# Kernel tuning notes

Measured on AMD Instinct MI355X. Metric: run time of the kernel, lower is better.

Reference implementation:

```python
import jax, jax.numpy as jnp
import numpy as np

B, S, D, H = 4, 2048, 1024, 16
HD = D // H  # 64
EPS = 1e-6


def _layernorm(x, scale, bias):
    mu = jnp.mean(x, axis=-1, keepdims=True)
    var = jnp.mean(jnp.square(x - mu), axis=-1, keepdims=True)
    return (x - mu) * jax.lax.rsqrt(var + EPS) * scale + bias


def setup_inputs() -> dict:
    key = jax.random.key(0)
    ks = jax.random.split(key, 10)
    s = 0.02
    return {
        "x": jax.random.normal(ks[0], (B, S, D), jnp.float32),
        "attention_mask": jnp.ones((B, 1, S, S), jnp.bool_),
        "eval": 1,
        "Wq": jax.random.normal(ks[1], (D, D), jnp.float32) * s,
        "bq": jnp.zeros((D,), jnp.float32),
        "Wk": jax.random.normal(ks[2], (D, D), jnp.float32) * s,
        "bk": jnp.zeros((D,), jnp.float32),
        "Wv": jax.random.normal(ks[3], (D, D), jnp.float32) * s,
        "bv": jnp.zeros((D,), jnp.float32),
        "Wo": jax.random.normal(ks[4], (D, D), jnp.float32) * s,
        "bo": jnp.zeros((D,), jnp.float32),
        "W1": jax.random.normal(ks[5], (D, D), jnp.float32) * s,
        "b1": jnp.zeros((D,), jnp.float32),
        "W2": jax.random.normal(ks[6], (D, D), jnp.float32) * s,
        "b2": jnp.zeros((D,), jnp.float32),
        "ln1_scale": jnp.ones((D,), jnp.float32),
        "ln1_bias": jnp.zeros((D,), jnp.float32),
        "ln2_scale": jnp.ones((D,), jnp.float32),
        "ln2_bias": jnp.zeros((D,), jnp.float32),
    }


def reference(x, attention_mask, eval, Wq, bq, Wk, bk, Wv, bv, Wo, bo,
              W1, b1, W2, b2, ln1_scale, ln1_bias, ln2_scale, ln2_bias):
    # --- MultiHeadAttention ---
    q = (x @ Wq + bq).reshape(B, S, H, HD)
    k = (x @ Wk + bk).reshape(B, S, H, HD)
    v = (x @ Wv + bv).reshape(B, S, H, HD)
    scores = jnp.einsum('bqhd,bkhd->bhqk', q, k) / jnp.sqrt(jnp.float32(HD))
    scores = jnp.where(attention_mask, scores, -jnp.inf)
    attn = jax.nn.softmax(scores, axis=-1)
    vals = jnp.einsum('bhqk,bkhd->bqhd', attn, v).reshape(B, S, D)
    attn_out = vals @ Wo + bo
    # --- residual + LN ---
    h = _layernorm(x + attn_out, ln1_scale, ln1_bias)
    # --- FeedForward (dropout deterministic -> identity) ---
    ff = jnp.maximum(h @ W1 + b1, 0.0) @ W2 + b2
    return _layernorm(h + ff, ln2_scale, ln2_bias)
```

## Files before the change

### kernel.cpp

```cpp
#include <hip/hip_runtime.h>

typedef __bf16 bf16;
typedef __bf16 bf16x8 __attribute__((ext_vector_type(8)));
typedef __bf16 bf16x4 __attribute__((ext_vector_type(4)));
typedef float f32x4 __attribute__((ext_vector_type(4)));
typedef float f32x16 __attribute__((ext_vector_type(16)));
typedef unsigned int uint;

#define BB 4
#define SS 2048
#define DD 1024
#define HH 16
#define HD 64
#define GM 8192
#define GN 1024
#define GK 1024
#define KVB 64
#define NT (SS / KVB)

__device__ __forceinline__ f32x4 mfma16(bf16x8 a, bf16x8 b, f32x4 c) {
    return __builtin_amdgcn_mfma_f32_16x16x32_bf16(a, b, c, 0, 0, 0);
}
__device__ __forceinline__ f32x16 mfma32(bf16x8 a, bf16x8 b, f32x16 c) {
    return __builtin_amdgcn_mfma_f32_32x32x16_bf16(a, b, c, 0, 0, 0);
}
__device__ __forceinline__ uint pack2(float x, float y) {
    union { bf16 b[2]; uint u; } uu;
    uu.b[0] = (bf16)x; uu.b[1] = (bf16)y;
    return uu.u;
}

__global__ __launch_bounds__(256) void cvt_kernel(const float* __restrict__ in, bf16* __restrict__ out, int n4) {
    int i = blockIdx.x * 256 + threadIdx.x;
    if (i < n4) {
        float4 v = *(const float4*)(in + (size_t)i * 4);
        bf16x4 o = {(bf16)v.x, (bf16)v.y, (bf16)v.z, (bf16)v.w};
        *(bf16x4*)(out + (size_t)i * 4) = o;
    }
}

__global__ __launch_bounds__(256) void wtrans_kernel(const float* __restrict__ W, bf16* __restrict__ Wt) {
    __shared__ float tile[64][65];
    const int t = threadIdx.x;
    const int k0 = blockIdx.x * 64, n0 = blockIdx.y * 64;
#pragma unroll
    for (int i = 0; i < 16; ++i) {
        int idx = i * 256 + t;
        int r = idx >> 6, c = idx & 63;
        tile[r][c] = W[(size_t)(k0 + r) * DD + n0 + c];
    }
    __syncthreads();
#pragma unroll
    for (int i = 0; i < 16; ++i) {
        int idx = i * 256 + t;
        int r = idx >> 6, c = idx & 63;
        Wt[(size_t)(n0 + r) * DD + k0 + c] = (bf16)tile[c][r];
    }
}

__global__ __launch_bounds__(256) void vtrans_kernel(const bf16* __restrict__ V, bf16* __restrict__ Vt) {
    __shared__ bf16 tile[64][72];
    const int t = threadIdx.x;
    const int bh = blockIdx.y;
    const int b = bh >> 4, h = bh & 15;
    const int s0 = blockIdx.x * 64;
#pragma unroll
    for (int i = 0; i < 16; ++i) {
        int idx = i * 256 + t;
        int r = idx >> 6, c = idx & 63;
        tile[r][c] = V[(size_t)(b * SS + s0 + r) * DD + h * HD + c];
    }
    __syncthreads();
#pragma unroll
    for (int i = 0; i < 16; ++i) {
        int idx = i * 256 + t;
        int r = idx >> 6, c = idx & 63;
        Vt[((size_t)bh * HD + r) * SS + s0 + c] = tile[c][r];
    }
}

template<bool OUTBF, bool RELU>
__global__ __launch_bounds__(256) void gemm_bt(const bf16* __restrict__ A, const bf16* __restrict__ Bt,
                                               const float* __restrict__ bias, void* __restrict__ C) {
    const int m0 = blockIdx.x * 128;
    const int n0 = blockIdx.y * 128;
    const int t = threadIdx.x;
    const int l = t & 63, wid = t >> 6;
    const int l16 = l & 15, g = l >> 4;
    const int wr = wid >> 1, wc = wid & 1;

    __shared__ int4 As4[512];
    __shared__ int4 Bs4[512];
    const char* Asc = (const char*)As4;
    const char* Bsc = (const char*)Bs4;

    const bf16* pa = A + (size_t)(m0 + (t >> 2)) * GK + (t & 3) * 8;
    const bf16* pb = Bt + (size_t)(n0 + (t >> 2)) * GK + (t & 3) * 8;
    int4 ra0 = *(const int4*)pa;
    int4 ra1 = *(const int4*)(pa + 64 * GK);
    int4 rb0 = *(const int4*)pb;
    int4 rb1 = *(const int4*)(pb + 64 * GK);

    f32x4 z = {0.f, 0.f, 0.f, 0.f};
    f32x4 acc[4][4];
#pragma unroll
    for (int mi = 0; mi < 4; ++mi)
#pragma unroll
        for (int ni = 0; ni < 4; ++ni) acc[mi][ni] = z;

    for (int kt = 0; kt < GK / 32; ++kt) {
        __syncthreads();
        As4[t] = ra0; As4[t + 256] = ra1;
        Bs4[t] = rb0; Bs4[t + 256] = rb1;
        __syncthreads();
        if (kt < GK / 32 - 1) {
            int off = (kt + 1) * 32;
            ra0 = *(const int4*)(pa + off);
            ra1 = *(const int4*)(pa + 64 * GK + off);
            rb0 = *(const int4*)(pb + off);
            rb1 = *(const int4*)(pb + 64 * GK + off);
        }
        bf16x8 af[4], bfr[4];
#pragma unroll
        for (int mi = 0; mi < 4; ++mi)
            af[mi] = *(const bf16x8*)(Asc + ((wr * 64 + mi * 16 + l16) * 32 + g * 8) * 2);
#pragma unroll
        for (int ni = 0; ni < 4; ++ni)
            bfr[ni] = *(const bf16x8*)(Bsc + ((wc * 64 + ni * 16 + l16) * 32 + g * 8) * 2);
#pragma unroll
        for (int mi = 0; mi < 4; ++mi)
#pragma unroll
            for (int ni = 0; ni < 4; ++ni)
                acc[mi][ni] = mfma16(af[mi], bfr[ni], acc[mi][ni]);
    }
#pragma unroll
    for (int ni = 0; ni < 4; ++ni) {
        const int col = n0 + wc * 64 + ni * 16 + l16;
        const float bv = bias[col];
#pragma unroll
        for (int mi = 0; mi < 4; ++mi) {
            const int row0 = m0 + wr * 64 + mi * 16 + g * 4;
#pragma unroll
            for (int j = 0; j < 4; ++j) {
                float v = acc[mi][ni][j] + bv;
                if (RELU) v = fmaxf(v, 0.f);
                if (OUTBF) ((bf16*)C)[(size_t)(row0 + j) * GN + col] = (bf16)v;
                else       ((float*)C)[(size_t)(row0 + j) * GN + col] = v;
            }
        }
    }
}

#define PFRAG(P, OFF, DST) { \
    uint a0 = pack2(P[OFF + 0], P[OFF + 1]); \
    uint a1 = pack2(P[OFF + 2], P[OFF + 3]); \
    uint a2 = pack2(P[OFF + 4], P[OFF + 5]); \
    uint a3 = pack2(P[OFF + 6], P[OFF + 7]); \
    uint s0 = (uint)__shfl_xor((int)a0, 32); \
    uint s1 = (uint)__shfl_xor((int)a1, 32); \
    uint s2 = (uint)__shfl_xor((int)a2, 32); \
    uint s3 = (uint)__shfl_xor((int)a3, 32); \
    union { uint u[4]; bf16x8 v; } uu; \
    uu.u[0] = lh ? s2 : a0; \
    uu.u[1] = lh ? s3 : a1; \
    uu.u[2] = lh ? a2 : s0; \
    uu.u[3] = lh ? a3 : s1; \
    DST = uu.v; }

__global__ __launch_bounds__(512) void attn_kernel(const bf16* __restrict__ Q, const bf16* __restrict__ K,
                                                   const bf16* __restrict__ Vt, bf16* __restrict__ vals) {
    const int wg = blockIdx.x;
    const int bh = wg >> 3;
    const int b = bh >> 4, h = bh & 15;
    const int q0 = (wg & 7) << 8;
    const int t = threadIdx.x;
    const int w = t >> 6, l = t & 63;
    const int l31 = l & 31, lh = l >> 5;
    const int qrow = q0 + w * 32 + l31;

    __shared__ int4 lds4[2048];
    char* lds = (char*)lds4;

    const float QS = 0.125f * 1.44269504f;
    const bf16* qp = Q + ((size_t)(b * SS + qrow)) * DD + h * HD + lh * 8;
    bf16x8 qf[4];
#pragma unroll
    for (int dc = 0; dc < 4; ++dc) {
        bf16x8 v = *(const bf16x8*)(qp + dc * 16);
#pragma unroll
        for (int j = 0; j < 8; ++j) v[j] = (bf16)((float)v[j] * QS);
        qf[dc] = v;
    }

    const int srow = t >> 3, schunk = t & 7;
    const bf16* kgp = K + ((size_t)(b * SS + srow)) * DD + h * HD + schunk * 8;
    const bf16* vgp = Vt + ((size_t)(bh * HD + srow)) * SS + schunk * 8;
    const int soff = srow * 128 + ((schunk * 16) ^ ((srow & 7) << 4));

    int4 rk = *(const int4*)kgp;
    int4 rv = *(const int4*)vgp;
    *(int4*)(lds + soff) = rk;
    *(int4*)(lds + 8192 + soff) = rv;

    const int sw = (l & 7) << 4;
    f32x16 o0, o1;
#pragma unroll
    for (int i = 0; i < 16; ++i) { o0[i] = 0.f; o1[i] = 0.f; }
    float m_run = -1e30f, l_run = 0.f;
    __syncthreads();

    for (int kt = 0; kt < NT; ++kt) {
        const int cur = (kt & 1) << 14;
        if (kt + 1 < NT) {
            rk = *(const int4*)(kgp + (size_t)(kt + 1) * KVB * DD);
            rv = *(const int4*)(vgp + (kt + 1) * KVB);
        }
        const char* kb = lds + cur;
        const char* vb = kb + 8192;
        f32x16 st0, st1;
#pragma unroll
        for (int i = 0; i < 16; ++i) { st0[i] = 0.f; st1[i] = 0.f; }
#pragma unroll
        for (int dc = 0; dc < 4; ++dc) {
            const int cb = (dc * 32 + lh * 16) ^ sw;
            bf16x8 ka0 = *(const bf16x8*)(kb + l31 * 128 + cb);
            bf16x8 ka1 = *(const bf16x8*)(kb + (32 + l31) * 128 + cb);
            st0 = mfma32(ka0, qf[dc], st0);
            st1 = mfma32(ka1, qf[dc], st1);
        }
        float mloc = st0[0];
#pragma unroll
        for (int i = 1; i < 16; ++i) mloc = fmaxf(mloc, st0[i]);
#pragma unroll
        for (int i = 0; i < 16; ++i) mloc = fmaxf(mloc, st1[i]);
        mloc = fmaxf(mloc, __shfl_xor(mloc, 32));
        if (!__all(mloc - m_run <= 11.0f)) {
            const float m_new = fmaxf(m_run, mloc);
            const float f = __builtin_amdgcn_exp2f(m_run - m_new);
            l_run *= f;
#pragma unroll
            for (int i = 0; i < 16; ++i) { o0[i] *= f; o1[i] *= f; }
            m_run = m_new;
        }
        float sum = 0.f;
#pragma unroll
        for (int i = 0; i < 16; ++i) { st0[i] = __builtin_amdgcn_exp2f(st0[i] - m_run); sum += st0[i]; }
#pragma unroll
        for (int i = 0; i < 16; ++i) { st1[i] = __builtin_amdgcn_exp2f(st1[i] - m_run); sum += st1[i]; }
        sum += __shfl_xor(sum, 32);
        l_run += sum;
        bf16x8 pf0, pf1, pf2, pf3;
        PFRAG(st0, 0, pf0); PFRAG(st0, 8, pf1); PFRAG(st1, 0, pf2); PFRAG(st1, 8, pf3);
#pragma unroll
        for (int dt = 0; dt < 2; ++dt) {
            const int rb = (dt * 32 + l31) * 128;
            f32x16 acc = dt ? o1 : o0;
            acc = mfma32(*(const bf16x8*)(vb + rb + ((0 * 32 + lh * 16) ^ sw)), pf0, acc);
            acc = mfma32(*(const bf16x8*)(vb + rb + ((1 * 32 + lh * 16) ^ sw)), pf1, acc);
            acc = mfma32(*(const bf16x8*)(vb + rb + ((2 * 32 + lh * 16) ^ sw)), pf2, acc);
            acc = mfma32(*(const bf16x8*)(vb + rb + ((3 * 32 + lh * 16) ^ sw)), pf3, acc);
            if (dt) o1 = acc; else o0 = acc;
        }
        if (kt + 1 < NT) {
            const int nxt = (~kt & 1) << 14;
            *(int4*)(lds + nxt + soff) = rk;
            *(int4*)(lds + nxt + 8192 + soff) = rv;
        }
        __syncthreads();
    }
    const float invl = 1.f / l_run;
    bf16* vp = vals + ((size_t)(b * SS + qrow)) * DD + h * HD;
#pragma unroll
    for (int dt = 0; dt < 2; ++dt) {
        const f32x16 oo = dt ? o1 : o0;
#pragma unroll
        for (int rg = 0; rg < 4; ++rg) {
            bf16x4 ov;
#pragma unroll
            for (int j = 0; j < 4; ++j) ov[j] = (bf16)(oo[rg * 4 + j] * invl);
            *(bf16x4*)(vp + dt * 32 + rg * 8 + lh * 4) = ov;
        }
    }
}

template<bool WB>
__global__ __launch_bounds__(256) void ln_kernel(const float* __restrict__ a, const float* __restrict__ b,
                                                 const float* __restrict__ scale, const float* __restrict__ bias,
                                                 float* __restrict__ outf, bf16* __restrict__ outb) {
    const int row = blockIdx.x;
    const int t = threadIdx.x;
    const size_t base = (size_t)row * DD + t * 4;
    const float4 va = *(const float4*)(a + base);
    const float4 vb = *(const float4*)(b + base);
    const float r0 = va.x + vb.x, r1 = va.y + vb.y, r2 = va.z + vb.z, r3 = va.w + vb.w;
    float s = r0 + r1 + r2 + r3;
    float q = r0 * r0 + r1 * r1 + r2 * r2 + r3 * r3;
#pragma unroll
    for (int d = 1; d < 64; d <<= 1) { s += __shfl_xor(s, d); q += __shfl_xor(q, d); }
    __shared__ float ss[4], qq[4];
    const int wid = t >> 6, l = t & 63;
    if (l == 0) { ss[wid] = s; qq[wid] = q; }
    __syncthreads();
    s = ss[0] + ss[1] + ss[2] + ss[3];
    q = qq[0] + qq[1] + qq[2] + qq[3];
    const float mean = s * (1.f / 1024.f);
    const float var = q * (1.f / 1024.f) - mean * mean;
    const float rstd = rsqrtf(var + 1e-6f);
    const float4 sc = *(const float4*)(scale + t * 4);
    const float4 bi = *(const float4*)(bias + t * 4);
    const float y0 = (r0 - mean) * rstd * sc.x + bi.x;
    const float y1 = (r1 - mean) * rstd * sc.y + bi.y;
    const float y2 = (r2 - mean) * rstd * sc.z + bi.z;
    const float y3 = (r3 - mean) * rstd * sc.w + bi.w;
    float4 yo; yo.x = y0; yo.y = y1; yo.z = y2; yo.w = y3;
    *(float4*)(outf + base) = yo;
    if (WB) {
        bf16x4 ob = {(bf16)y0, (bf16)y1, (bf16)y2, (bf16)y3};
        *(bf16x4*)(outb + base) = ob;
    }
}

extern "C" void kernel_launch(void* const* d_in, const int* in_sizes, int n_in,
                              void* d_out, int out_size, void* d_ws, size_t ws_size,
                              hipStream_t stream) {
    const float* x   = (const float*)d_in[0];
    const float* Wq  = (const float*)d_in[3];  const float* bq = (const float*)d_in[4];
    const float* Wk  = (const float*)d_in[5];  const float* bk = (const float*)d_in[6];
    const float* Wv  = (const float*)d_in[7];  const float* bv = (const float*)d_in[8];
    const float* Wo  = (const float*)d_in[9];  const float* bo = (const float*)d_in[10];
    const float* W1  = (const float*)d_in[11]; const float* b1 = (const float*)d_in[12];
    const float* W2  = (const float*)d_in[13]; const float* b2 = (const float*)d_in[14];
    const float* l1s = (const float*)d_in[15]; const float* l1b = (const float*)d_in[16];
    const float* l2s = (const float*)d_in[17]; const float* l2b = (const float*)d_in[18];

    char* ws = (char*)d_ws;
    bf16* WTq = (bf16*)ws;
    bf16* WTk = WTq + (1 << 20);
    bf16* WTv = WTq + 2 * (1 << 20);
    bf16* WTo = WTq + 3 * (1 << 20);
    bf16* WT1 = WTq + 4 * (1 << 20);
    bf16* WT2 = WTq + 5 * (1 << 20);
    char* A1 = ws + 12582912;
    char* A2 = A1 + 16777216;
    char* A3 = A2 + 16777216;
    char* A4 = A3 + 16777216;
    char* A5 = A4 + 16777216;

    bf16*  xb      = (bf16*)A1;
    bf16*  Qb      = (bf16*)A2;
    bf16*  Kb      = (bf16*)A3;
    bf16*  Vb      = (bf16*)A4;
    bf16*  Vt      = (bf16*)A5;
    bf16*  valsb   = (bf16*)A4;
    float* attnout = (float*)A2;
    float* h       = (float*)A5;
    bf16*  hb      = (bf16*)A4;
    bf16*  ff1b    = (bf16*)A1;
    float* ff2     = (float*)A2;
    float* out     = (float*)d_out;

    const dim3 blk(256);
    const dim3 ggrid(GM / 128, GN / 128);

    wtrans_kernel<<<dim3(16, 16), blk, 0, stream>>>(Wq, WTq);
    wtrans_kernel<<<dim3(16, 16), blk, 0, stream>>>(Wk, WTk);
    wtrans_kernel<<<dim3(16, 16), blk, 0, stream>>>(Wv, WTv);
    wtrans_kernel<<<dim3(16, 16), blk, 0, stream>>>(Wo, WTo);
    wtrans_kernel<<<dim3(16, 16), blk, 0, stream>>>(W1, WT1);
    wtrans_kernel<<<dim3(16, 16), blk, 0, stream>>>(W2, WT2);
    cvt_kernel<<<8192, blk, 0, stream>>>(x, xb, GM * DD / 4);
    gemm_bt<true, false><<<ggrid, blk, 0, stream>>>(xb, WTq, bq, Qb);
    gemm_bt<true, false><<<ggrid, blk, 0, stream>>>(xb, WTk, bk, Kb);
    gemm_bt<true, false><<<ggrid, blk, 0, stream>>>(xb, WTv, bv, Vb);
    vtrans_kernel<<<dim3(SS / 64, BB * HH), blk, 0, stream>>>(Vb, Vt);
    attn_kernel<<<BB * HH * (SS / 256), 512, 0, stream>>>(Qb, Kb, Vt, valsb);
    gemm_bt<false, false><<<ggrid, blk, 0, stream>>>(valsb, WTo, bo, attnout);
    ln_kernel<true><<<GM, blk, 0, stream>>>(x, attnout, l1s, l1b, h, hb);
    gemm_bt<true, true><<<ggrid, blk, 0, stream>>>(hb, WT1, b1, ff1b);
    gemm_bt<false, false><<<ggrid, blk, 0, stream>>>(ff1b, WT2, b2, ff2);
    ln_kernel<false><<<GM, blk, 0, stream>>>(h, ff2, l2s, l2b, out, nullptr);
}
```

Before: 486.6 us.

## Use direct global-to-LDS loads with double buffering in GEMM, raise MFMA priority in attention

```diff
diff --git a/kernel.cpp b/kernel.cpp
--- a/kernel.cpp
+++ b/kernel.cpp
@@ -29,6 +29,10 @@
     uu.b[0] = (bf16)x; uu.b[1] = (bf16)y;
     return uu.u;
 }
+__device__ __forceinline__ void gload16(const bf16* g, char* l) {
+    __builtin_amdgcn_global_load_lds((const __attribute__((address_space(1))) void*)g,
+                                     (__attribute__((address_space(3))) void*)l, 16, 0, 0);
+}
 
 __global__ __launch_bounds__(256) void cvt_kernel(const float* __restrict__ in, bf16* __restrict__ out, int n4) {
     int i = blockIdx.x * 256 + threadIdx.x;
@@ -89,17 +93,17 @@
     const int l16 = l & 15, g = l >> 4;
     const int wr = wid >> 1, wc = wid & 1;
 
-    __shared__ int4 As4[512];
-    __shared__ int4 Bs4[512];
-    const char* Asc = (const char*)As4;
-    const char* Bsc = (const char*)Bs4;
+    __shared__ char smem[32768];
 
     const bf16* pa = A + (size_t)(m0 + (t >> 2)) * GK + (t & 3) * 8;
     const bf16* pb = Bt + (size_t)(n0 + (t >> 2)) * GK + (t & 3) * 8;
-    int4 ra0 = *(const int4*)pa;
-    int4 ra1 = *(const int4*)(pa + 64 * GK);
-    int4 rb0 = *(const int4*)pb;
-    int4 rb1 = *(const int4*)(pb + 64 * GK);
+    char* lpa = smem + t * 16;
+    char* lpb = smem + 8192 + t * 16;
+
+    gload16(pa, lpa);
+    gload16(pa + 64 * GK, lpa + 4096);
+    gload16(pb, lpb);
+    gload16(pb + 64 * GK, lpb + 4096);
 
     f32x4 z = {0.f, 0.f, 0.f, 0.f};
     f32x4 acc[4][4];
@@ -108,30 +112,33 @@
 #pragma unroll
         for (int ni = 0; ni < 4; ++ni) acc[mi][ni] = z;
 
+    __syncthreads();
+
     for (int kt = 0; kt < GK / 32; ++kt) {
-        __syncthreads();
-        As4[t] = ra0; As4[t + 256] = ra1;
-        Bs4[t] = rb0; Bs4[t + 256] = rb1;
-        __syncthreads();
-        if (kt < GK / 32 - 1) {
-            int off = (kt + 1) * 32;
-            ra0 = *(const int4*)(pa + off);
-            ra1 = *(const int4*)(pa + 64 * GK + off);
-            rb0 = *(const int4*)(pb + off);
-            rb1 = *(const int4*)(pb + 64 * GK + off);
-        }
+        const int cur = (kt & 1) << 14;
+        if (kt + 1 < GK / 32) {
+            const int nxt = 16384 - cur;
+            const int off = (kt + 1) * 32;
+            gload16(pa + off, lpa + nxt);
+            gload16(pa + 64 * GK + off, lpa + nxt + 4096);
+            gload16(pb + off, lpb + nxt);
+            gload16(pb + 64 * GK + off, lpb + nxt + 4096);
+        }
+        const char* Asc = smem + cur;
+        const char* Bsc = smem + cur + 8192;
         bf16x8 af[4], bfr[4];
 #pragma unroll
         for (int mi = 0; mi < 4; ++mi)
-            af[mi] = *(const bf16x8*)(Asc + ((wr * 64 + mi * 16 + l16) * 32 + g * 8) * 2);
+            af[mi] = *(const bf16x8*)(Asc + (wr * 64 + mi * 16 + l16) * 64 + g * 16);
 #pragma unroll
         for (int ni = 0; ni < 4; ++ni)
-            bfr[ni] = *(const bf16x8*)(Bsc + ((wc * 64 + ni * 16 + l16) * 32 + g * 8) * 2);
+            bfr[ni] = *(const bf16x8*)(Bsc + (wc * 64 + ni * 16 + l16) * 64 + g * 16);
 #pragma unroll
         for (int mi = 0; mi < 4; ++mi)
 #pragma unroll
             for (int ni = 0; ni < 4; ++ni)
                 acc[mi][ni] = mfma16(af[mi], bfr[ni], acc[mi][ni]);
+        __syncthreads();
     }
 #pragma unroll
     for (int ni = 0; ni < 4; ++ni) {
@@ -220,6 +227,7 @@
         f32x16 st0, st1;
 #pragma unroll
         for (int i = 0; i < 16; ++i) { st0[i] = 0.f; st1[i] = 0.f; }
+        __builtin_amdgcn_s_setprio(1);
 #pragma unroll
         for (int dc = 0; dc < 4; ++dc) {
             const int cb = (dc * 32 + lh * 16) ^ sw;
@@ -228,6 +236,7 @@
             st0 = mfma32(ka0, qf[dc], st0);
             st1 = mfma32(ka1, qf[dc], st1);
         }
+        __builtin_amdgcn_s_setprio(0);
         float mloc = st0[0];
 #pragma unroll
         for (int i = 1; i < 16; ++i) mloc = fmaxf(mloc, st0[i]);
@@ -251,6 +260,7 @@
         l_run += sum;
         bf16x8 pf0, pf1, pf2, pf3;
         PFRAG(st0, 0, pf0); PFRAG(st0, 8, pf1); PFRAG(st1, 0, pf2); PFRAG(st1, 8, pf3);
+        __builtin_amdgcn_s_setprio(1);
 #pragma unroll
         for (int dt = 0; dt < 2; ++dt) {
             const int rb = (dt * 32 + l31) * 128;
@@ -261,6 +271,7 @@
             acc = mfma32(*(const bf16x8*)(vb + rb + ((3 * 32 + lh * 16) ^ sw)), pf3, acc);
             if (dt) o1 = acc; else o0 = acc;
         }
+        __builtin_amdgcn_s_setprio(0);
         if (kt + 1 < NT) {
             const int nxt = (~kt & 1) << 14;
             *(int4*)(lds + nxt + soff) = rk;
```

After: 475.1 us. 1.02x faster.
